# Kernel optimization log

Hardware: AMD Instinct MI355X
Metric: run time of the kernel (lower is better)

## Reference

```python
import jax, jax.numpy as jnp
import numpy as np
import math

B, T, D = 4, 2048, 1024
H, DK, DV = 4, 128, 256
KD, VD = H * DK, H * DV
LOG_T_REF = math.log(512.0)
EPS = 1e-5


def setup_inputs() -> dict:
    key = jax.random.key(0)
    ks = jax.random.split(key, 8)
    hs = jax.random.normal(ks[0], (B, T, D), dtype=jnp.float32)
    Wq = jax.random.normal(ks[1], (KD, D), dtype=jnp.float32) / math.sqrt(D)
    Wk = jax.random.normal(ks[2], (KD, D), dtype=jnp.float32) / math.sqrt(D)
    Wv = jax.random.normal(ks[3], (VD, D), dtype=jnp.float32) / math.sqrt(D)
    Wg = jax.random.normal(ks[4], (VD, D), dtype=jnp.float32) / math.sqrt(D)
    Wa = jax.random.normal(ks[5], (KD, D), dtype=jnp.float32) / math.sqrt(D)
    Wo = jax.random.normal(ks[6], (D, VD), dtype=jnp.float32) / math.sqrt(VD)
    # _post_init: A_log_base = 0, A_log_delta = log(exp(gap)-1+1e-6), gap = log(16)/(H-1)
    gap = math.log(16.0) / (H - 1)
    A_log_base = jnp.zeros((), dtype=jnp.float32)
    A_log_delta = jnp.full((H - 1,), math.log(math.exp(gap) - 1.0 + 1e-6), dtype=jnp.float32)
    # dt_bias init (inverse-softplus of dt sampled loguniform in [1e-3, 1e-1])
    rng = np.random.default_rng(0)
    dt = np.exp(rng.random(KD) * (math.log(0.1) - math.log(0.001)) + math.log(0.001))
    dt = np.clip(dt, 1e-4, None)
    dt_bias = jnp.asarray(dt + np.log(-np.expm1(-dt)), dtype=jnp.float32)
    g_norm_weight = jnp.ones((VD,), dtype=jnp.float32)
    return {"hidden_states": hs, "Wq": Wq, "Wk": Wk, "Wv": Wv, "Wg": Wg, "Wa": Wa,
            "Wo": Wo, "A_log_base": A_log_base, "A_log_delta": A_log_delta,
            "dt_bias": dt_bias, "g_norm_weight": g_norm_weight}


def _gla_forward(hidden_states, Wq, Wk, Wv, Wg, Wa, Wo, A_log_base, A_log_delta, dt_bias, g_norm_weight):
    b, t, _ = hidden_states.shape
    q = (hidden_states @ Wq.T).reshape(b, t, H, DK)
    k = (hidden_states @ Wk.T).reshape(b, t, H, DK)
    v = (hidden_states @ Wv.T).reshape(b, t, H, DV)
    a = (hidden_states @ Wa.T).reshape(b, t, H, DK)

    # geometric spectral allocation: A_log[h] = base + cumsum(softplus(delta))
    A_log = A_log_base + jnp.concatenate([jnp.zeros((1,), dtype=A_log_delta.dtype),
                                          jnp.cumsum(jax.nn.softplus(A_log_delta))])
    # per-head log-decay gate: gk = -exp(A_log) * softplus(a + dt_bias)  [b,t,h,dk]
    gk = -jnp.exp(A_log)[None, None, :, None] * jax.nn.softplus(a + dt_bias.reshape(H, DK)[None, None])

    # analytical position-adaptive alpha
    cum = A_log - A_log[0]
    kk = jnp.arange(H, dtype=A_log.dtype)
    mean_gap = cum[-1] / (H - 1)
    taper = (H - 1 - kk) / (H - 1)
    alpha = jnp.clip(taper + (cum - kk * mean_gap) / LOG_T_REF, 0.0, 1.0)  # [H]
    pos = jnp.arange(1, t + 1, dtype=jnp.float32)
    gk = gk * (pos[:, None] ** (-alpha[None, :]))[None, :, :, None]

    # gated linear attention recurrence: S_t = exp(gk_t)*S_{t-1} + k_t^T v_t ; o_t = q_t S_t
    scale = DK ** -0.5
    qT = jnp.moveaxis(q, 1, 0) * scale  # [t,b,h,dk]
    kT = jnp.moveaxis(k, 1, 0)
    vT = jnp.moveaxis(v, 1, 0)
    gT = jnp.moveaxis(gk, 1, 0)

    def step(S, inp):
        qt, kt, vt, gt = inp
        S = S * jnp.exp(gt)[..., None] + kt[..., None] * vt[..., None, :]  # [b,h,dk,dv]
        ot = jnp.einsum('bhk,bhkv->bhv', qt, S)
        return S, ot

    S0 = jnp.zeros((b, H, DK, DV), dtype=jnp.float32)
    _, oT = jax.lax.scan(step, S0, (qT, kT, vT, gT))
    o = jnp.moveaxis(oT, 0, 1)  # [b,t,h,dv]

    # fused RMSNorm + swish output gate (per head over dv)
    g = (hidden_states @ Wg.T).reshape(b, t, H, DV)
    o = o * jax.lax.rsqrt(jnp.mean(o * o, axis=-1, keepdims=True) + EPS)
    o = o * g_norm_weight.reshape(H, DV)[None, None] * (g * jax.nn.sigmoid(g))
    return o.reshape(b, t, VD) @ Wo.T


def reference(hidden_states, Wq, Wk, Wv, Wg, Wa, Wo, A_log_base, A_log_delta, dt_bias, g_norm_weight):
    return _gla_forward(hidden_states, Wq, Wk, Wv, Wg, Wa, Wo, A_log_base, A_log_delta, dt_bias, g_norm_weight)
```

## Files before the change

kernel.cpp:

```cpp
#include <hip/hip_runtime.h>
#include <math.h>

#define Bn   4
#define Tn   2048
#define Dn   1024
#define Hn   4
#define DKn  128
#define DVn  256
#define KDn  512
#define VDn  1024
#define NROWS 8192
#define NCC  32
#define CLEN 64
#define LOG_T_REF_F 6.2383246250395075f

using bf16x8 = __attribute__((ext_vector_type(8))) short;
using f32x4  = __attribute__((ext_vector_type(4))) float;

__device__ __forceinline__ float softplus_f(float x) {
    return fmaxf(x, 0.0f) + log1pf(expf(-fabsf(x)));
}
__device__ __forceinline__ ushort f2bf(float f) {
    unsigned u = __float_as_uint(f);
    u = (u + 0x7fffu + ((u >> 16) & 1u)) >> 16;
    return (ushort)u;
}
__device__ __forceinline__ float bf2f(ushort u) {
    return __uint_as_float((unsigned)u << 16);
}
__device__ __forceinline__ void gload16(const void* g, void* l) {
    __builtin_amdgcn_global_load_lds(
        (const __attribute__((address_space(1))) unsigned*)g,
        (__attribute__((address_space(3))) unsigned*)l, 16, 0, 0);
}

struct CastArgs {
    const float* src[7];
    ushort* dst[7];
    int cum[8];
};
__global__ __launch_bounds__(256) void cast_all(CastArgs a) {
    const int total = a.cum[7];
    for (int i = blockIdx.x * 256 + threadIdx.x; i < total; i += gridDim.x * 256) {
        int s = 0;
        #pragma unroll
        for (int k = 1; k < 7; ++k) s += (i >= a.cum[k]) ? 1 : 0;
        const int off = i - a.cum[s];
        float4 v = *(const float4*)&a.src[s][(size_t)off * 4];
        ushort4 u;
        u.x = f2bf(v.x); u.y = f2bf(v.y); u.z = f2bf(v.z); u.w = f2bf(v.w);
        *(ushort4*)&a.dst[s][(size_t)off * 4] = u;
    }
}

template<int MODE, int NX>
__global__ __launch_bounds__(256) void mm2(const ushort* __restrict__ A,
    const ushort* __restrict__ Bw, float* __restrict__ C,
    ushort* __restrict__ C2, float* __restrict__ Eo,
    const float* __restrict__ dt_bias, const float* __restrict__ A_log_base,
    const float* __restrict__ A_log_delta)
{
    __shared__ __align__(16) ushort As[4][128][8];
    __shared__ __align__(16) ushort Bs[4][128][8];
    const int raw = blockIdx.x;
    const int nwg = NX * 64;
    const int l = (raw & 7) * (nwg >> 3) + (raw >> 3);
    const int bx = l % NX, by = l / NX;
    const int tid = threadIdx.x;
    const int lane = tid & 63, w = tid >> 6;
    const int l15 = lane & 15, lg = lane >> 4;
    const int wr = (w >> 1) << 6, wc = (w & 1) << 6;
    const int row0 = by << 7, col0 = bx << 7;

    const ushort* Ag0 = A  + (size_t)(row0 + lane) * Dn + w * 8;
    const ushort* Ag1 = A  + (size_t)(row0 + 64 + lane) * Dn + w * 8;
    const ushort* Bg0 = Bw + (size_t)(col0 + lane) * Dn + w * 8;
    const ushort* Bg1 = Bw + (size_t)(col0 + 64 + lane) * Dn + w * 8;
    ushort* lA0 = &As[w][0][0];
    ushort* lA1 = &As[w][64][0];
    ushort* lB0 = &Bs[w][0][0];
    ushort* lB1 = &Bs[w][64][0];

    f32x4 acc[4][4];
    #pragma unroll
    for (int m = 0; m < 4; ++m)
        #pragma unroll
        for (int n = 0; n < 4; ++n)
            acc[m][n] = (f32x4){0.f, 0.f, 0.f, 0.f};

    for (int kt = 0; kt < Dn; kt += 32) {
        __syncthreads();
        gload16(Ag0 + kt, lA0);
        gload16(Ag1 + kt, lA1);
        gload16(Bg0 + kt, lB0);
        gload16(Bg1 + kt, lB1);
        __syncthreads();
        bf16x8 af[4], bv[4];
        #pragma unroll
        for (int m = 0; m < 4; ++m) af[m] = *(const bf16x8*)&As[lg][wr + m*16 + l15][0];
        #pragma unroll
        for (int n = 0; n < 4; ++n) bv[n] = *(const bf16x8*)&Bs[lg][wc + n*16 + l15][0];
        #pragma unroll
        for (int m = 0; m < 4; ++m)
            #pragma unroll
            for (int n = 0; n < 4; ++n)
                acc[m][n] = __builtin_amdgcn_mfma_f32_16x16x32_bf16(af[m], bv[n], acc[m][n], 0, 0, 0);
    }

    if (MODE == 1 && col0 >= 1024) {
        const float base_ = A_log_base[0];
        const float s0 = softplus_f(A_log_delta[0]);
        const float s1 = softplus_f(A_log_delta[1]);
        const float s2 = softplus_f(A_log_delta[2]);
        const float c3 = s0 + s1 + s2;
        const float mg = c3 * (1.0f / 3.0f);
        float pf[4][4];
        #pragma unroll
        for (int m = 0; m < 4; ++m) {
            const int row = row0 + wr + m * 16 + lg * 4;
            #pragma unroll
            for (int r = 0; r < 4; ++r) {
                const int t = (row + r) & (Tn - 1);
                pf[m][r] = logf((float)(t + 1));
            }
        }
        #pragma unroll
        for (int n = 0; n < 4; ++n) {
            const int dk = col0 - 1024 + wc + n * 16 + l15;
            const int h = dk >> 7;
            const float cumh = (h == 0) ? 0.f : (h == 1) ? s0 : (h == 2) ? s0 + s1 : c3;
            float alpha = (float)(3 - h) * (1.0f / 3.0f)
                        + (cumh - (float)h * mg) * (1.0f / LOG_T_REF_F);
            alpha = fminf(fmaxf(alpha, 0.0f), 1.0f);
            const float expA = expf(base_ + cumh);
            const float db = dt_bias[dk];
            #pragma unroll
            for (int m = 0; m < 4; ++m) {
                const int row = row0 + wr + m * 16 + lg * 4;
                #pragma unroll
                for (int r = 0; r < 4; ++r) {
                    const float p = expf(-alpha * pf[m][r]);
                    Eo[(size_t)(row + r) * KDn + dk] =
                        -expA * softplus_f(acc[m][n][r] + db) * p;
                }
            }
        }
    } else if (MODE == 2 && col0 >= 1024) {
        #pragma unroll
        for (int m = 0; m < 4; ++m) {
            const int row = row0 + wr + m * 16 + lg * 4;
            #pragma unroll
            for (int n = 0; n < 4; ++n) {
                const int col = col0 - 1024 + wc + n * 16 + l15;
                #pragma unroll
                for (int r = 0; r < 4; ++r)
                    C2[(size_t)(row + r) * 1024 + col] = f2bf(acc[m][n][r]);
            }
        }
    } else {
        const float s = (MODE == 1 && col0 < 512) ? 0.08838834764831845f : 1.0f;
        #pragma unroll
        for (int m = 0; m < 4; ++m) {
            const int row = row0 + wr + m * 16 + lg * 4;
            #pragma unroll
            for (int n = 0; n < 4; ++n) {
                const int col = col0 + wc + n * 16 + l15;
                #pragma unroll
                for (int r = 0; r < 4; ++r)
                    C[(size_t)(row + r) * 1024 + col] = acc[m][n][r] * s;
            }
        }
    }
}

__global__ __launch_bounds__(1024) void gla_chunk(
    float* qk, const float* __restrict__ Gb, const float* __restrict__ vb,
    float* __restrict__ o, float* __restrict__ Sl, float* __restrict__ Dc)
{
    extern __shared__ __align__(16) char smem[];
    float*  g    = (float*)smem;
    ushort* qraw = (ushort*)(smem + 33792);
    ushort* kraw = (ushort*)(smem + 51200);
    ushort* Qb   = (ushort*)(smem + 68608);
    ushort* Koff = (ushort*)(smem + 86016);
    ushort* KhT  = (ushort*)(smem + 112128);
    ushort* At   = (ushort*)(smem + 130560);
    ushort* VT   = (ushort*)smem;
    float*  qsum = (float*)(smem + 86016);

    const int bid = blockIdx.x;
    const int co = bid >> 4, bh = bid & 15;
    const int b = bh >> 2, h = bh & 3;
    const int tid = threadIdx.x;
    const int w = tid >> 6, lane = tid & 63;
    const int l15 = lane & 15, lg = lane >> 4;
    const size_t rowbase = (size_t)(b * Tn + co * CLEN);

    float c16[16];
    int dk1 = 0, qr1 = 0;
    if (tid < 512) {
        dk1 = tid & 127; qr1 = tid >> 7;
        const float* gp = Gb + (rowbase + qr1 * 16) * 512 + h * 128 + dk1;
        float run = 0.f;
        #pragma unroll
        for (int s = 0; s < 16; ++s) { run += gp[(size_t)s * 512]; c16[s] = run; }
        qsum[qr1 * 128 + dk1] = run;
    }
    __syncthreads();
    if (tid < 512) {
        float pre = 0.f;
        for (int r = 0; r < qr1; ++r) pre += qsum[r * 128 + dk1];
        #pragma unroll
        for (int s = 0; s < 16; ++s) g[(qr1 * 16 + s) * 132 + dk1] = c16[s] + pre;
    }
    __syncthreads();

    #pragma unroll
    for (int it = 0; it < 8; ++it) {
        const int idx = tid + it * 1024;
        const int t = idx >> 7, dk = idx & 127;
        const float gi = g[t * 132 + dk];
        const size_t qaddr = (rowbase + t) * 1024 + h * 128 + dk;
        const float qv = qk[qaddr];
        const float gr = (t < 16) ? 0.f : g[(16 * (t >> 4) - 1) * 132 + dk];
        Qb[t * 136 + dk] = f2bf(qv * __expf(gi - gr));
        qraw[t * 136 + dk] = f2bf(qv);
        qk[qaddr] = qv * __expf(gi);
        const float kv = qk[qaddr + 512];
        kraw[t * 136 + dk] = f2bf(kv);
        KhT[dk * 72 + t] = f2bf(kv * __expf(g[63 * 132 + dk] - gi));
        if (t < 16) Koff[t * 136 + dk]        = f2bf(kv * __expf(g[15 * 132 + dk] - gi));
        if (t < 32) Koff[(16 + t) * 136 + dk] = f2bf(kv * __expf(g[31 * 132 + dk] - gi));
        if (t < 48) Koff[(48 + t) * 136 + dk] = f2bf(kv * __expf(g[47 * 132 + dk] - gi));
    }
    for (int i = tid; i < 2304; i += 1024) ((int*)At)[i] = 0;
    if (tid < 128)
        Dc[(co * 16 + bh) * 128 + tid] = __expf(g[63 * 132 + tid]);
    __syncthreads();

    if (w < 6) {
        const int Tt[6] = {16, 32, 32, 48, 48, 48};
        const int Ss[6] = { 0,  0, 16,  0, 16, 32};
        const int Kb[6] = { 0, 16, 16, 48, 48, 48};
        const int T = Tt[w], S = Ss[w], KB = Kb[w];
        f32x4 acc = (f32x4){0.f, 0.f, 0.f, 0.f};
        #pragma unroll
        for (int kk = 0; kk < 4; ++kk) {
            bf16x8 a  = *(const bf16x8*)&Qb[(T + l15) * 136 + kk * 32 + lg * 8];
            bf16x8 bb = *(const bf16x8*)&Koff[(KB + S + l15) * 136 + kk * 32 + lg * 8];
            acc = __builtin_amdgcn_mfma_f32_16x16x32_bf16(a, bb, acc, 0, 0, 0);
        }
        #pragma unroll
        for (int r = 0; r < 4; ++r)
            At[(T + lg * 4 + r) * 72 + S + l15] = f2bf(acc[r]);
    } else if (w < 14) {
        const int d = (w - 6) >> 1, hf = (w - 6) & 1;
        #pragma unroll
        for (int pp = 0; pp < 2; ++pp) {
            const int p = hf * 128 + pp * 64 + lane;
            const int i_ = p >> 4, j_ = p & 15;
            if (j_ <= i_) {
                const int ti = d * 16 + i_, tj = d * 16 + j_;
                float a = 0.f;
                for (int dk = 0; dk < 128; ++dk) {
                    const float qf = bf2f(qraw[ti * 136 + dk]);
                    const float kf = bf2f(kraw[tj * 136 + dk]);
                    a += qf * kf * __expf(g[ti * 132 + dk] - g[tj * 132 + dk]);
                }
                At[ti * 72 + tj] = f2bf(a);
            }
        }
    }
    __syncthreads();

    {
        const int dv4 = (tid & 63) * 4, tseg = tid >> 6;
        float4 vv[4];
        #pragma unroll
        for (int s = 0; s < 4; ++s)
            vv[s] = *(const float4*)&vb[(rowbase + tseg * 4 + s) * 1024 + h * 256 + dv4];
        const float* vf = (const float*)vv;
        #pragma unroll
        for (int c = 0; c < 4; ++c) {
            int lo = (unsigned)f2bf(vf[0 * 4 + c]) | ((unsigned)f2bf(vf[1 * 4 + c]) << 16);
            int hi = (unsigned)f2bf(vf[2 * 4 + c]) | ((unsigned)f2bf(vf[3 * 4 + c]) << 16);
            *(int2*)((char*)VT + (size_t)(dv4 + c) * 144 + tseg * 8) = make_int2(lo, hi);
        }
    }
    __syncthreads();

    float* sp = Sl + (((size_t)co * 16 + bh) << 15);
    for (int id = w; id < 192; id += 16) {
        if (id < 64) {
            const int mt = id >> 4, nt = id & 15;
            f32x4 acc = (f32x4){0.f, 0.f, 0.f, 0.f};
            #pragma unroll
            for (int kk = 0; kk < 2; ++kk) {
                bf16x8 a  = *(const bf16x8*)&At[(mt * 16 + l15) * 72 + kk * 32 + lg * 8];
                bf16x8 bb = *(const bf16x8*)&VT[(nt * 16 + l15) * 72 + kk * 32 + lg * 8];
                acc = __builtin_amdgcn_mfma_f32_16x16x32_bf16(a, bb, acc, 0, 0, 0);
            }
            #pragma unroll
            for (int r = 0; r < 4; ++r)
                o[(rowbase + mt * 16 + lg * 4 + r) * 1024 + h * 256 + nt * 16 + l15] = acc[r];
        } else {
            const int sid = id - 64;
            const int mt = sid >> 4, nt = sid & 15;
            f32x4 acc = (f32x4){0.f, 0.f, 0.f, 0.f};
            #pragma unroll
            for (int kk = 0; kk < 2; ++kk) {
                bf16x8 a  = *(const bf16x8*)&KhT[(mt * 16 + l15) * 72 + kk * 32 + lg * 8];
                bf16x8 bb = *(const bf16x8*)&VT[(nt * 16 + l15) * 72 + kk * 32 + lg * 8];
                acc = __builtin_amdgcn_mfma_f32_16x16x32_bf16(a, bb, acc, 0, 0, 0);
            }
            #pragma unroll
            for (int r = 0; r < 4; ++r)
                sp[(size_t)(mt * 16 + lg * 4 + r) * 256 + nt * 16 + l15] = acc[r];
        }
    }
}

__global__ __launch_bounds__(256) void combine(float* __restrict__ Sl,
                                               const float* __restrict__ Dc) {
    const int bh = blockIdx.y;
    const int e4 = blockIdx.x * 256 + threadIdx.x;
    const int dk = e4 >> 6;
    float4 s = make_float4(0.f, 0.f, 0.f, 0.f);
    #pragma unroll 4
    for (int c = 0; c < NCC; ++c) {
        float4* p = (float4*)(Sl + (((size_t)c * 16 + bh) << 15)) + e4;
        float4 local = *p;
        const float d = Dc[(c * 16 + bh) * DKn + dk];
        *p = s;
        s.x = s.x * d + local.x;  s.y = s.y * d + local.y;
        s.z = s.z * d + local.z;  s.w = s.w * d + local.w;
    }
}

__global__ __launch_bounds__(256, 4) void fixup(const float* __restrict__ qt,
    const float* __restrict__ Sl, float* __restrict__ o)
{
    __shared__ __align__(16) float Aq[16][68];
    __shared__ __align__(16) float Bs[16][68];
    const int raw = blockIdx.x;
    const int l = (raw & 7) * 256 + (raw >> 3);
    const int dvt = l & 3, bh = (l >> 2) & 15, co = l >> 6;
    const int b = bh >> 2, h = bh & 3;
    const int tid = threadIdx.x;
    const int tx = tid & 15, ty = tid >> 4;
    const int t0 = co * CLEN;
    const int dv0 = dvt * 64;

    const float* qbase = qt + (size_t)(b * Tn + t0) * 1024 + h * 128;
    const float* sbase = Sl + (((size_t)co * 16 + bh) << 15) + dv0;

    float acc[4][4] = {};
    for (int k0 = 0; k0 < DKn; k0 += 16) {
        __syncthreads();
        {
            const int t = tid >> 2, kk4 = (tid & 3) << 2;
            float4 a = *(const float4*)&qbase[(size_t)t * 1024 + k0 + kk4];
            Aq[kk4 + 0][t] = a.x; Aq[kk4 + 1][t] = a.y;
            Aq[kk4 + 2][t] = a.z; Aq[kk4 + 3][t] = a.w;
        }
        {
            const int dk = tid >> 4, dvq = (tid & 15) << 2;
            *(float4*)&Bs[dk][dvq] = *(const float4*)&sbase[(size_t)(k0 + dk) * 256 + dvq];
        }
        __syncthreads();
        #pragma unroll
        for (int kk = 0; kk < 16; ++kk) {
            float4 a  = *(const float4*)&Aq[kk][ty * 4];
            float4 bv = *(const float4*)&Bs[kk][tx * 4];
            float ar[4] = {a.x, a.y, a.z, a.w};
            float br[4] = {bv.x, bv.y, bv.z, bv.w};
            #pragma unroll
            for (int i = 0; i < 4; ++i)
                #pragma unroll
                for (int j = 0; j < 4; ++j)
                    acc[i][j] += ar[i] * br[j];
        }
    }
    float* obp = o + (size_t)(b * Tn + t0) * 1024 + h * 256 + dv0;
    #pragma unroll
    for (int i = 0; i < 4; ++i) {
        float* row = obp + (size_t)(ty * 4 + i) * 1024 + tx * 4;
        float4 c = *(float4*)row;
        c.x += acc[i][0]; c.y += acc[i][1];
        c.z += acc[i][2]; c.w += acc[i][3];
        *(float4*)row = c;
    }
}

__global__ __launch_bounds__(256) void rms_gate(const float* __restrict__ o,
    const ushort* __restrict__ gbf, const float* __restrict__ wt,
    ushort* __restrict__ obf)
{
    const int tid = threadIdx.x;
    const int w = tid >> 6, lane = tid & 63;
    const int row = blockIdx.x * 4 + w;
    const int n = row >> 2, h = row & 3;
    const size_t ob_base = (size_t)n * VDn + h * DVn + lane * 4;

    float4 o4 = *(const float4*)&o[ob_base];
    float ss = o4.x*o4.x + o4.y*o4.y + o4.z*o4.z + o4.w*o4.w;
    #pragma unroll
    for (int m = 1; m < 64; m <<= 1) ss += __shfl_xor(ss, m);
    const float r = rsqrtf(ss * (1.0f / DVn) + 1e-5f);

    ushort4 gu = *(const ushort4*)&gbf[ob_base];
    float gx = bf2f(gu.x), gy = bf2f(gu.y), gz = bf2f(gu.z), gw = bf2f(gu.w);
    float4 w4 = *(const float4*)&wt[h * DVn + lane * 4];
    ushort4 u;
    u.x = f2bf(o4.x * r * w4.x * (gx / (1.0f + expf(-gx))));
    u.y = f2bf(o4.y * r * w4.y * (gy / (1.0f + expf(-gy))));
    u.z = f2bf(o4.z * r * w4.z * (gz / (1.0f + expf(-gz))));
    u.w = f2bf(o4.w * r * w4.w * (gw / (1.0f + expf(-gw))));
    *(ushort4*)&obf[ob_base] = u;
}

extern "C" void kernel_launch(void* const* d_in, const int* in_sizes, int n_in,
                              void* d_out, int out_size, void* d_ws, size_t ws_size,
                              hipStream_t stream) {
    const float* hs          = (const float*)d_in[0];
    const float* Wq          = (const float*)d_in[1];
    const float* Wk          = (const float*)d_in[2];
    const float* Wv          = (const float*)d_in[3];
    const float* Wg          = (const float*)d_in[4];
    const float* Wa          = (const float*)d_in[5];
    const float* Wo          = (const float*)d_in[6];
    const float* A_log_base  = (const float*)d_in[7];
    const float* A_log_delta = (const float*)d_in[8];
    const float* dt_bias     = (const float*)d_in[9];
    const float* gnw         = (const float*)d_in[10];
    float* out = (float*)d_out;

    char* ws = (char*)d_ws;
    float*  qk   = (float*)(ws);
    float*  vb   = (float*)(ws + ((size_t)32  << 20));
    float*  Gbuf = (float*)(ws + ((size_t)64  << 20));
    float*  Sl   = (float*)(ws + ((size_t)80  << 20));
    float*  ob   = (float*)(ws + ((size_t)144 << 20));
    ushort* hsb  = (ushort*)(ws + ((size_t)144 << 20));
    ushort* gbf  = (ushort*)(ws + ((size_t)176 << 20));
    ushort* Wqkab= (ushort*)(ws + ((size_t)192 << 20));
    ushort* Wvgb = (ushort*)(ws + ((size_t)195 << 20));
    ushort* Wob  = (ushort*)(ws + ((size_t)199 << 20));
    float*  Dc   = (float*)(ws + ((size_t)201 << 20));
    ushort* obf  = (ushort*)qk;

    CastArgs ca;
    ca.src[0] = hs; ca.src[1] = Wq; ca.src[2] = Wk; ca.src[3] = Wa;
    ca.src[4] = Wv; ca.src[5] = Wg; ca.src[6] = Wo;
    ca.dst[0] = hsb;
    ca.dst[1] = Wqkab;
    ca.dst[2] = Wqkab + KDn * Dn;
    ca.dst[3] = Wqkab + 2 * KDn * Dn;
    ca.dst[4] = Wvgb;
    ca.dst[5] = Wvgb + VDn * Dn;
    ca.dst[6] = Wob;
    const int n4s[7] = {NROWS * Dn / 4, KDn * Dn / 4, KDn * Dn / 4, KDn * Dn / 4,
                        VDn * Dn / 4, VDn * Dn / 4, VDn * Dn / 4};
    ca.cum[0] = 0;
    for (int i = 0; i < 7; ++i) ca.cum[i + 1] = ca.cum[i] + n4s[i];
    cast_all<<<2048, 256, 0, stream>>>(ca);

    mm2<1,12><<<768,  256, 0, stream>>>(hsb, Wqkab, qk, nullptr, Gbuf,
                                        dt_bias, A_log_base, A_log_delta);
    mm2<2,16><<<1024, 256, 0, stream>>>(hsb, Wvgb, vb, gbf, nullptr,
                                        nullptr, nullptr, nullptr);

    (void)hipFuncSetAttribute((const void*)gla_chunk,
                              hipFuncAttributeMaxDynamicSharedMemorySize, 139776);
    gla_chunk<<<512, 1024, 139776, stream>>>(qk, Gbuf, vb, ob, Sl, Dc);
    combine<<<dim3(32, 16), 256, 0, stream>>>(Sl, Dc);
    fixup<<<2048, 256, 0, stream>>>(qk, Sl, ob);

    rms_gate<<<NROWS * Hn / 4, 256, 0, stream>>>(ob, gbf, gnw, obf);
    mm2<0,8><<<512, 256, 0, stream>>>(obf, Wob, out, nullptr, nullptr,
                                      nullptr, nullptr, nullptr);
}
```

Measured before the change: 322.8 us.

## Merge QKA and VG projection GEMMs into one launch with 64-wide K tiles

Concatenates Wq, Wk, Wa, Wv and Wg into one bf16 weight buffer and runs a single GEMM launch. Each column block routes its epilogue to q/k scaling, the decay gate, the fp32 v output or the bf16 gate output. The K loop now stages 64 elements per barrier pair instead of 32, which halves the synchronisations and doubles LDS use. The intent is to remove a launch and its tail, and to cut barrier overhead, at the cost of more shared memory per block.

```diff
diff --git a/kernel.cpp b/kernel.cpp
--- a/kernel.cpp
+++ b/kernel.cpp
@@ -54,14 +54,14 @@
 }
 
 template<int MODE, int NX>
-__global__ __launch_bounds__(256) void mm2(const ushort* __restrict__ A,
+__global__ __launch_bounds__(256) void mm3(const ushort* __restrict__ A,
     const ushort* __restrict__ Bw, float* __restrict__ C,
-    ushort* __restrict__ C2, float* __restrict__ Eo,
+    float* __restrict__ Cv, ushort* __restrict__ C2, float* __restrict__ Eo,
     const float* __restrict__ dt_bias, const float* __restrict__ A_log_base,
     const float* __restrict__ A_log_delta)
 {
-    __shared__ __align__(16) ushort As[4][128][8];
-    __shared__ __align__(16) ushort Bs[4][128][8];
+    __shared__ __align__(16) ushort As[8][128][8];
+    __shared__ __align__(16) ushort Bs[8][128][8];
     const int raw = blockIdx.x;
     const int nwg = NX * 64;
     const int l = (raw & 7) * (nwg >> 3) + (raw >> 3);
@@ -72,14 +72,10 @@
     const int wr = (w >> 1) << 6, wc = (w & 1) << 6;
     const int row0 = by << 7, col0 = bx << 7;
 
-    const ushort* Ag0 = A  + (size_t)(row0 + lane) * Dn + w * 8;
-    const ushort* Ag1 = A  + (size_t)(row0 + 64 + lane) * Dn + w * 8;
-    const ushort* Bg0 = Bw + (size_t)(col0 + lane) * Dn + w * 8;
-    const ushort* Bg1 = Bw + (size_t)(col0 + 64 + lane) * Dn + w * 8;
-    ushort* lA0 = &As[w][0][0];
-    ushort* lA1 = &As[w][64][0];
-    ushort* lB0 = &Bs[w][0][0];
-    ushort* lB1 = &Bs[w][64][0];
+    const ushort* A0 = A  + (size_t)(row0 + lane) * Dn + w * 8;
+    const ushort* A1 = A  + (size_t)(row0 + 64 + lane) * Dn + w * 8;
+    const ushort* B0 = Bw + (size_t)(col0 + lane) * Dn + w * 8;
+    const ushort* B1 = Bw + (size_t)(col0 + 64 + lane) * Dn + w * 8;
 
     f32x4 acc[4][4];
     #pragma unroll
@@ -88,26 +84,35 @@
         for (int n = 0; n < 4; ++n)
             acc[m][n] = (f32x4){0.f, 0.f, 0.f, 0.f};
 
-    for (int kt = 0; kt < Dn; kt += 32) {
+    for (int kt = 0; kt < Dn; kt += 64) {
         __syncthreads();
-        gload16(Ag0 + kt, lA0);
-        gload16(Ag1 + kt, lA1);
-        gload16(Bg0 + kt, lB0);
-        gload16(Bg1 + kt, lB1);
+        gload16(A0 + kt,      &As[w][0][0]);
+        gload16(A0 + kt + 32, &As[w + 4][0][0]);
+        gload16(A1 + kt,      &As[w][64][0]);
+        gload16(A1 + kt + 32, &As[w + 4][64][0]);
+        gload16(B0 + kt,      &Bs[w][0][0]);
+        gload16(B0 + kt + 32, &Bs[w + 4][0][0]);
+        gload16(B1 + kt,      &Bs[w][64][0]);
+        gload16(B1 + kt + 32, &Bs[w + 4][64][0]);
         __syncthreads();
-        bf16x8 af[4], bv[4];
-        #pragma unroll
-        for (int m = 0; m < 4; ++m) af[m] = *(const bf16x8*)&As[lg][wr + m*16 + l15][0];
-        #pragma unroll
-        for (int n = 0; n < 4; ++n) bv[n] = *(const bf16x8*)&Bs[lg][wc + n*16 + l15][0];
-        #pragma unroll
-        for (int m = 0; m < 4; ++m)
+        #pragma unroll
+        for (int ks = 0; ks < 2; ++ks) {
+            bf16x8 af[4], bv[4];
+            #pragma unroll
+            for (int m = 0; m < 4; ++m)
+                af[m] = *(const bf16x8*)&As[ks * 4 + lg][wr + m * 16 + l15][0];
             #pragma unroll
             for (int n = 0; n < 4; ++n)
-                acc[m][n] = __builtin_amdgcn_mfma_f32_16x16x32_bf16(af[m], bv[n], acc[m][n], 0, 0, 0);
-    }
-
-    if (MODE == 1 && col0 >= 1024) {
+                bv[n] = *(const bf16x8*)&Bs[ks * 4 + lg][wc + n * 16 + l15][0];
+            #pragma unroll
+            for (int m = 0; m < 4; ++m)
+                #pragma unroll
+                for (int n = 0; n < 4; ++n)
+                    acc[m][n] = __builtin_amdgcn_mfma_f32_16x16x32_bf16(af[m], bv[n], acc[m][n], 0, 0, 0);
+        }
+    }
+
+    if (MODE == 1 && col0 >= 1024 && col0 < 1536) {
         const float base_ = A_log_base[0];
         const float s0 = softplus_f(A_log_delta[0]);
         const float s1 = softplus_f(A_log_delta[1]);
@@ -145,16 +150,31 @@
                 }
             }
         }
-    } else if (MODE == 2 && col0 >= 1024) {
-        #pragma unroll
-        for (int m = 0; m < 4; ++m) {
-            const int row = row0 + wr + m * 16 + lg * 4;
-            #pragma unroll
-            for (int n = 0; n < 4; ++n) {
-                const int col = col0 - 1024 + wc + n * 16 + l15;
-                #pragma unroll
-                for (int r = 0; r < 4; ++r)
-                    C2[(size_t)(row + r) * 1024 + col] = f2bf(acc[m][n][r]);
+    } else if (MODE == 1 && col0 >= 1536) {
+        const int cv0 = col0 - 1536;
+        if (cv0 < 1024) {
+            #pragma unroll
+            for (int m = 0; m < 4; ++m) {
+                const int row = row0 + wr + m * 16 + lg * 4;
+                #pragma unroll
+                for (int n = 0; n < 4; ++n) {
+                    const int col = cv0 + wc + n * 16 + l15;
+                    #pragma unroll
+                    for (int r = 0; r < 4; ++r)
+                        Cv[(size_t)(row + r) * 1024 + col] = acc[m][n][r];
+                }
+            }
+        } else {
+            #pragma unroll
+            for (int m = 0; m < 4; ++m) {
+                const int row = row0 + wr + m * 16 + lg * 4;
+                #pragma unroll
+                for (int n = 0; n < 4; ++n) {
+                    const int col = cv0 - 1024 + wc + n * 16 + l15;
+                    #pragma unroll
+                    for (int r = 0; r < 4; ++r)
+                        C2[(size_t)(row + r) * 1024 + col] = f2bf(acc[m][n][r]);
+                }
             }
         }
     } else {
@@ -443,8 +463,7 @@
     float*  ob   = (float*)(ws + ((size_t)144 << 20));
     ushort* hsb  = (ushort*)(ws + ((size_t)144 << 20));
     ushort* gbf  = (ushort*)(ws + ((size_t)176 << 20));
-    ushort* Wqkab= (ushort*)(ws + ((size_t)192 << 20));
-    ushort* Wvgb = (ushort*)(ws + ((size_t)195 << 20));
+    ushort* Wcat = (ushort*)(ws + ((size_t)192 << 20));
     ushort* Wob  = (ushort*)(ws + ((size_t)199 << 20));
     float*  Dc   = (float*)(ws + ((size_t)201 << 20));
     ushort* obf  = (ushort*)qk;
@@ -453,11 +472,11 @@
     ca.src[0] = hs; ca.src[1] = Wq; ca.src[2] = Wk; ca.src[3] = Wa;
     ca.src[4] = Wv; ca.src[5] = Wg; ca.src[6] = Wo;
     ca.dst[0] = hsb;
-    ca.dst[1] = Wqkab;
-    ca.dst[2] = Wqkab + KDn * Dn;
-    ca.dst[3] = Wqkab + 2 * KDn * Dn;
-    ca.dst[4] = Wvgb;
-    ca.dst[5] = Wvgb + VDn * Dn;
+    ca.dst[1] = Wcat;
+    ca.dst[2] = Wcat + (size_t)512 * 1024;
+    ca.dst[3] = Wcat + (size_t)1024 * 1024;
+    ca.dst[4] = Wcat + (size_t)1536 * 1024;
+    ca.dst[5] = Wcat + (size_t)2560 * 1024;
     ca.dst[6] = Wob;
     const int n4s[7] = {NROWS * Dn / 4, KDn * Dn / 4, KDn * Dn / 4, KDn * Dn / 4,
                         VDn * Dn / 4, VDn * Dn / 4, VDn * Dn / 4};
@@ -465,10 +484,8 @@
     for (int i = 0; i < 7; ++i) ca.cum[i + 1] = ca.cum[i] + n4s[i];
     cast_all<<<2048, 256, 0, stream>>>(ca);
 
-    mm2<1,12><<<768,  256, 0, stream>>>(hsb, Wqkab, qk, nullptr, Gbuf,
+    mm3<1,28><<<1792, 256, 0, stream>>>(hsb, Wcat, qk, vb, gbf, Gbuf,
                                         dt_bias, A_log_base, A_log_delta);
-    mm2<2,16><<<1024, 256, 0, stream>>>(hsb, Wvgb, vb, gbf, nullptr,
-                                        nullptr, nullptr, nullptr);
 
     (void)hipFuncSetAttribute((const void*)gla_chunk,
                               hipFuncAttributeMaxDynamicSharedMemorySize, 139776);
@@ -477,6 +494,6 @@
     fixup<<<2048, 256, 0, stream>>>(qk, Sl, ob);
 
     rms_gate<<<NROWS * Hn / 4, 256, 0, stream>>>(ob, gbf, gnw, obf);
-    mm2<0,8><<<512, 256, 0, stream>>>(obf, Wob, out, nullptr, nullptr,
+    mm3<0,8><<<512, 256, 0, stream>>>(obf, Wob, out, nullptr, nullptr, nullptr,
                                       nullptr, nullptr, nullptr);
 }
```

Result: faster. 309.1 us (-4.3%).
